# Optimization experiments

Measured on AMD Instinct MI355X. Metric: run time of the kernel, lower is better.

Reference implementation:

```python
import jax, jax.numpy as jnp
import numpy as np

HIDDEN = 2048
ENGRAM = 256
ENTRIES = 32768
K = 3  # conv kernel size
LN_EPS = 1e-6
NORM_EPS = 1e-8
INV_TEMP = ENGRAM ** 0.5  # retrieval_temperature = 1/sqrt(engram_dim)
CLAMP_MIN = 0.5  # step 0 < clamp_until_step=800 -> hard clamp active


def _l2norm(x):
    n = jnp.linalg.norm(x, axis=-1, keepdims=True)
    return x / jnp.maximum(n, NORM_EPS)


def _rmsnorm(x, w, eps=LN_EPS):
    ms = jnp.mean(jnp.square(x), axis=-1, keepdims=True)
    return x * jax.lax.rsqrt(ms + eps) * w


def _layernorm(x, g, b, eps=LN_EPS):
    mu = jnp.mean(x, axis=-1, keepdims=True)
    var = jnp.mean(jnp.square(x - mu), axis=-1, keepdims=True)
    return (x - mu) * jax.lax.rsqrt(var + eps) * g + b


def setup_inputs() -> dict:
    key = jax.random.key(0)
    ks = jax.random.split(key, 7)
    s = lambda fan: 1.0 / np.sqrt(fan)
    return {
        "hidden_state": jax.random.normal(ks[0], (4, 1024, HIDDEN), jnp.float32),
        "table": jax.random.normal(ks[1], (ENTRIES, ENGRAM), jnp.float32),
        "Wq": jax.random.normal(ks[2], (HIDDEN, ENGRAM), jnp.float32) * s(HIDDEN),
        "ln_gamma": jnp.ones((ENGRAM,), jnp.float32),
        "ln_beta": jnp.zeros((ENGRAM,), jnp.float32),
        "Wk": jax.random.normal(ks[3], (ENGRAM, HIDDEN), jnp.float32) * s(ENGRAM),
        "Wv": jax.random.normal(ks[4], (ENGRAM, HIDDEN), jnp.float32) * s(ENGRAM),
        "gate_norm_w": jnp.ones((HIDDEN,), jnp.float32),
        "key_norm_w": jnp.ones((HIDDEN,), jnp.float32),
        # depthwise causal conv weight [C, K] (torch init zeros; randn for a meaningful test)
        "conv_w": jax.random.normal(ks[5], (HIDDEN, K), jnp.float32) * 0.1,
    }


def reference(hidden_state, table, Wq, ln_gamma, ln_beta, Wk, Wv,
              gate_norm_w, key_norm_w, conv_w):
    B, L, C = hidden_state.shape
    # --- retrieval: cosine-sim softmax attention over frozen table ---
    q = jnp.einsum('blc,ce->ble', hidden_state, Wq)
    qn = _l2norm(q)
    tn = _l2norm(table)
    sims = jnp.einsum('ble,te->blt', qn, tn)            # [B,L,T]
    weights = jax.nn.softmax(sims * INV_TEMP, axis=-1)
    retrieved = jnp.einsum('blt,te->ble', weights, table)
    retrieved = _layernorm(retrieved, ln_gamma, ln_beta)
    # --- key/value projections + gating ---
    key_ = jnp.einsum('ble,ec->blc', retrieved, Wk)
    value = jnp.einsum('ble,ec->blc', retrieved, Wv)
    h_norm = _rmsnorm(hidden_state, gate_norm_w)
    k_norm = _rmsnorm(key_, key_norm_w)
    dot = jnp.sum(h_norm * k_norm, axis=-1, keepdims=True)
    raw_gate = jax.nn.sigmoid(dot / np.sqrt(C).astype(np.float32))
    gate = jnp.maximum(raw_gate, CLAMP_MIN)             # clamp phase (step < 800)
    gated = gate * value                                 # [B,L,C]
    # --- causal depthwise conv along seq (left pad K-1) ---
    padded = jnp.pad(gated, ((0, 0), (K - 1, 0), (0, 0)))
    conv = sum(conv_w[:, k] * padded[:, k:k + L, :] for k in range(K))
    return jax.nn.silu(conv), gate
```

## Files before the change

### kernel.cpp

```cpp
#include <hip/hip_runtime.h>
#include <stdint.h>


#define NTOK 4096
#define CDIM 2048
#define EDIM 256
#define TROWS 32768
#define SPLIT 16
#define OUT0 (NTOK * CDIM)

typedef __attribute__((ext_vector_type(8))) short bf16x8;
typedef __attribute__((ext_vector_type(4))) float f32x4;

__device__ inline float bf2f(unsigned short u) { return __uint_as_float((unsigned)u << 16); }
__device__ inline unsigned short f2bf(float f) {
  unsigned x = __float_as_uint(f);
  x += 0x7fffu + ((x >> 16) & 1u);
  return (unsigned short)(x >> 16);
}
__device__ inline unsigned cvt_pk_bf16(float lo, float hi) {
  unsigned r;
  asm("v_cvt_pk_bf16_f32 %0, %1, %2" : "=v"(r) : "v"(lo), "v"(hi));
  return r;
}
__device__ inline void gll16(const void* g, void* l) {
  __builtin_amdgcn_global_load_lds((const __attribute__((address_space(1))) void*)g,
                                   (__attribute__((address_space(3))) void*)l, 16, 0, 0);
}
#define WAIT_VM0() do { asm volatile("s_waitcnt vmcnt(0)" ::: "memory"); \
                        __builtin_amdgcn_sched_barrier(0); } while (0)
#define WAIT_LGKM0() do { asm volatile("s_waitcnt lgkmcnt(0)" ::: "memory"); \
                          __builtin_amdgcn_sched_barrier(0); } while (0)
#define BARRIER() do { __builtin_amdgcn_s_barrier(); \
                       __builtin_amdgcn_sched_barrier(0); } while (0)

__global__ __launch_bounds__(256) void cast_bf16_kernel(
    const float* __restrict__ in, unsigned short* __restrict__ out) {
  const int idx = blockIdx.x * 256 + threadIdx.x;
  float4 v0 = *reinterpret_cast<const float4*>(&in[(size_t)idx * 8]);
  float4 v1 = *reinterpret_cast<const float4*>(&in[(size_t)idx * 8 + 4]);
  bf16x8 o;
  o[0] = (short)f2bf(v0.x); o[1] = (short)f2bf(v0.y);
  o[2] = (short)f2bf(v0.z); o[3] = (short)f2bf(v0.w);
  o[4] = (short)f2bf(v1.x); o[5] = (short)f2bf(v1.y);
  o[6] = (short)f2bf(v1.z); o[7] = (short)f2bf(v1.w);
  *reinterpret_cast<bf16x8*>(&out[(size_t)idx * 8]) = o;
}

__global__ __launch_bounds__(256) void transpose_cast_kernel(
    const float* __restrict__ in0, const float* __restrict__ in1,
    unsigned short* __restrict__ out, int R, int C) {
  __shared__ float lt[32][33];
  const int tid = threadIdx.x;
  const int r0 = blockIdx.x * 32, c0 = blockIdx.y * 32;
  const float* in = blockIdx.z ? in1 : in0;
  unsigned short* op = out + (size_t)blockIdx.z * R * C;
  {
    int r = tid >> 3, c4 = (tid & 7) * 4;
    float4 v = *reinterpret_cast<const float4*>(&in[(size_t)(r0 + r) * C + c0 + c4]);
    lt[r][c4] = v.x; lt[r][c4 + 1] = v.y; lt[r][c4 + 2] = v.z; lt[r][c4 + 3] = v.w;
  }
  __syncthreads();
  {
    int c = tid >> 3, r4 = (tid & 7) * 4;
#pragma unroll
    for (int j = 0; j < 4; ++j)
      op[(size_t)(c0 + c) * R + r0 + r4 + j] = f2bf(lt[r4 + j][c]);
  }
}

__global__ __launch_bounds__(256) void tabprep_kernel(
    const float* __restrict__ table, unsigned short* __restrict__ tnb,
    unsigned short* __restrict__ tvb) {
  __shared__ float lt[32][257];
  __shared__ float inv[32];
  const int tid = threadIdx.x, nb = blockIdx.x;
  const int r0 = nb * 32;
#pragma unroll
  for (int i = 0; i < 8; ++i) {
    int id = i * 256 + tid;
    int row = id >> 6, e4 = (id & 63) * 4;
    float4 v = *reinterpret_cast<const float4*>(&table[(size_t)(r0 + row) * EDIM + e4]);
    lt[row][e4] = v.x; lt[row][e4 + 1] = v.y; lt[row][e4 + 2] = v.z; lt[row][e4 + 3] = v.w;
  }
  __syncthreads();
  {
    int row = tid >> 3, sub = tid & 7;
    float ss = 0.f;
#pragma unroll
    for (int j = 0; j < 32; ++j) { float v = lt[row][sub + 8 * j]; ss = fmaf(v, v, ss); }
    ss += __shfl_xor(ss, 1); ss += __shfl_xor(ss, 2); ss += __shfl_xor(ss, 4);
    if (sub == 0) inv[row] = 1.f / fmaxf(sqrtf(ss), 1e-8f);
  }
  __syncthreads();
#pragma unroll
  for (int i = 0; i < 4; ++i) {
    int q = i * 256 + tid;
    {
      int c8 = q >> 5, row = q & 31;
      bf16x8 v;
#pragma unroll
      for (int j = 0; j < 8; ++j) v[j] = (short)f2bf(lt[row][c8 * 8 + j] * inv[row]);
      *reinterpret_cast<bf16x8*>(&tnb[(size_t)nb * 8192 + q * 8]) = v;
    }
    {
      int hi = q >> 8, e = q & 255;
      bf16x8 v;
#pragma unroll
      for (int j = 0; j < 8; ++j) v[j] = (short)f2bf(lt[hi * 8 + j][e]);
      *reinterpret_cast<bf16x8*>(&tvb[(size_t)nb * 8192 + q * 8]) = v;
    }
  }
}

template <bool F32OUT>
__global__ __launch_bounds__(256, 2) void gemm_bt_kernel(
    const unsigned short* __restrict__ A, const unsigned short* __restrict__ BT,
    void* __restrict__ Cout, int M, int N, int Kfull, int klen) {
  __shared__ alignas(16) unsigned short sA[2][128 * 64];
  __shared__ alignas(16) unsigned short sB[2][128 * 64];
  const int tid = threadIdx.x;
  const int lane = tid & 63;
  const int wave = tid >> 6;
  const int laneLo = lane & 15, laneHi = lane >> 4;
  const int nbn = N >> 7;
  const int bm = blockIdx.x / nbn, bn = blockIdx.x % nbn;
  const int koff = blockIdx.y * klen;
  const int wr = wave >> 1, wc = wave & 1;
  f32x4 acc[4][4];
#pragma unroll
  for (int m = 0; m < 4; ++m)
#pragma unroll
    for (int n = 0; n < 4; ++n) acc[m][n] = (f32x4){0.f, 0.f, 0.f, 0.f};
  const int nkt = klen >> 6;
  auto STAGE = [&](int b, int kt) {
#pragma unroll
    for (int i = 0; i < 4; ++i) {
      int q = i * 256 + tid;
      int row = q >> 3, cl = q & 7;
      int cs = cl ^ (row & 7);
      gll16(A + ((size_t)(bm * 128 + row) * Kfull + koff + kt * 64 + cs * 8), &sA[b][q * 8]);
      gll16(BT + ((size_t)(bn * 128 + row) * Kfull + koff + kt * 64 + cs * 8), &sB[b][q * 8]);
    }
  };
  STAGE(0, 0);
  for (int kt = 0; kt < nkt; ++kt) {
    __syncthreads();
    if (kt + 1 < nkt) STAGE((kt & 1) ^ 1, kt + 1);
    const unsigned short* pA = sA[kt & 1];
    const unsigned short* pB = sB[kt & 1];
#pragma unroll
    for (int ks = 0; ks < 2; ++ks) {
      bf16x8 af[4], bfr[4];
#pragma unroll
      for (int m = 0; m < 4; ++m) {
        int row = wr * 64 + m * 16 + laneLo;
        af[m] = *reinterpret_cast<const bf16x8*>(&pA[(row * 8 + ((ks * 4 + laneHi) ^ (row & 7))) * 8]);
      }
#pragma unroll
      for (int n = 0; n < 4; ++n) {
        int row = wc * 64 + n * 16 + laneLo;
        bfr[n] = *reinterpret_cast<const bf16x8*>(&pB[(row * 8 + ((ks * 4 + laneHi) ^ (row & 7))) * 8]);
      }
#pragma unroll
      for (int m = 0; m < 4; ++m)
#pragma unroll
        for (int n = 0; n < 4; ++n)
          acc[m][n] = __builtin_amdgcn_mfma_f32_16x16x32_bf16(af[m], bfr[n], acc[m][n], 0, 0, 0);
    }
  }
#pragma unroll
  for (int m = 0; m < 4; ++m)
#pragma unroll
    for (int n = 0; n < 4; ++n)
#pragma unroll
      for (int r = 0; r < 4; ++r) {
        size_t idx = (size_t)(bm * 128 + wr * 64 + m * 16 + laneHi * 4 + r) * N +
                     bn * 128 + wc * 64 + n * 16 + laneLo;
        if (F32OUT)
          ((float*)Cout)[(size_t)blockIdx.y * M * N + idx] = acc[m][n][r];
        else
          ((unsigned short*)Cout)[idx] = f2bf(acc[m][n][r]);
      }
}

__global__ __launch_bounds__(256) void qcombine_kernel(
    const float* __restrict__ qpart, unsigned short* __restrict__ qn) {
  __shared__ float red[4];
  const int t = blockIdx.x, e = threadIdx.x;
  const int wave = e >> 6, lane = e & 63;
  float v = qpart[(size_t)t * EDIM + e] + qpart[((size_t)NTOK + t) * EDIM + e];
  float ss = v * v;
#pragma unroll
  for (int m = 1; m <= 32; m <<= 1) ss += __shfl_xor(ss, m);
  if (lane == 0) red[wave] = ss;
  __syncthreads();
  ss = red[0] + red[1] + red[2] + red[3];
  const float inv = 1.f / fmaxf(sqrtf(ss), 1e-8f);
  qn[(size_t)t * EDIM + e] = f2bf(v * inv);
}

__global__ __launch_bounds__(512, 2) void attn_kernel(
    const unsigned short* __restrict__ qn, const unsigned short* __restrict__ tnb,
    const unsigned short* __restrict__ tvb, unsigned short* __restrict__ Opart,
    float* __restrict__ lpart) {
  __shared__ alignas(16) unsigned short bufK[2][8192];
  __shared__ alignas(16) unsigned short bufV[2][8192];
  __shared__ alignas(16) unsigned short pbuf[16][16][40];
  const int tid = threadIdx.x;
  const int wave = tid >> 6, lane = tid & 63;
  const int Lo = lane & 15, Hi = lane >> 4;
  const int cid = (blockIdx.x & 7) * 32 + (blockIdx.x >> 3);
  const int split = cid >> 4, tb = cid & 15;
  const int qkBase = tb * 256 + wave * 32;
  bf16x8 qf[2][8];
#pragma unroll
  for (int g = 0; g < 2; ++g)
#pragma unroll
    for (int ks = 0; ks < 8; ++ks)
      qf[g][ks] = *reinterpret_cast<const bf16x8*>(
          qn + (size_t)(qkBase + g * 16 + Lo) * EDIM + ks * 32 + Hi * 8);
  const int pvG = (wave & 3) * 4;
  const int pvF = (wave >> 2) * 8;
  f32x4 o[4][8];
#pragma unroll
  for (int ng = 0; ng < 4; ++ng)
#pragma unroll
    for (int f = 0; f < 8; ++f) o[ng][f] = (f32x4){0.f, 0.f, 0.f, 0.f};
  float l_run[2] = {0.f, 0.f};
  const int nt = (TROWS / SPLIT) / 32;
  const int nb0 = split * nt;
  auto STAGE = [&](int b, int blk) {
#pragma unroll
    for (int i = 0; i < 2; ++i) {
      gll16(tnb + (size_t)blk * 8192 + (i * 512 + tid) * 8, &bufK[b][(i * 512 + tid) * 8]);
      gll16(tvb + (size_t)blk * 8192 + (i * 512 + tid) * 8, &bufV[b][(i * 512 + tid) * 8]);
    }
  };
  STAGE(0, nb0);
  for (int it = 0; it < nt; ++it) {
    const int cur = it & 1;
    WAIT_VM0();
    WAIT_LGKM0();
    BARRIER();
    if (it + 1 < nt) STAGE(cur ^ 1, nb0 + it + 1);
    f32x4 z00 = {0.f, 0.f, 0.f, 0.f}, z01 = z00, z10 = z00, z11 = z00;
    __builtin_amdgcn_s_setprio(1);
#pragma unroll
    for (int ks = 0; ks < 8; ++ks) {
      bf16x8 a0 = *reinterpret_cast<const bf16x8*>(&bufK[cur][((ks * 4 + Hi) * 32 + Lo) * 8]);
      bf16x8 a1 = *reinterpret_cast<const bf16x8*>(&bufK[cur][((ks * 4 + Hi) * 32 + 16 + Lo) * 8]);
      z00 = __builtin_amdgcn_mfma_f32_16x16x32_bf16(a0, qf[0][ks], z00, 0, 0, 0);
      z01 = __builtin_amdgcn_mfma_f32_16x16x32_bf16(a1, qf[0][ks], z01, 0, 0, 0);
      z10 = __builtin_amdgcn_mfma_f32_16x16x32_bf16(a0, qf[1][ks], z10, 0, 0, 0);
      z11 = __builtin_amdgcn_mfma_f32_16x16x32_bf16(a1, qf[1][ks], z11, 0, 0, 0);
    }
    __builtin_amdgcn_s_setprio(0);
#pragma unroll
    for (int g = 0; g < 2; ++g) {
      const f32x4 za = g ? z10 : z00;
      const f32x4 zb = g ? z11 : z01;
      float p[8];
#pragma unroll
      for (int r = 0; r < 4; ++r) {
        p[r] = __expf(fmaf(16.f, za[r], -16.f));
        p[4 + r] = __expf(fmaf(16.f, zb[r], -16.f));
      }
      l_run[g] += ((p[0] + p[1]) + (p[2] + p[3])) + ((p[4] + p[5]) + (p[6] + p[7]));
      unsigned short* pb = &pbuf[wave * 2 + g][Lo][0];
      *reinterpret_cast<uint2*>(pb + Hi * 4) =
          make_uint2(cvt_pk_bf16(p[0], p[1]), cvt_pk_bf16(p[2], p[3]));
      *reinterpret_cast<uint2*>(pb + 16 + Hi * 4) =
          make_uint2(cvt_pk_bf16(p[4], p[5]), cvt_pk_bf16(p[6], p[7]));
    }
    WAIT_LGKM0();
    BARRIER();
    bf16x8 pa0 = *reinterpret_cast<const bf16x8*>(&pbuf[pvG + 0][Lo][Hi * 8]);
    bf16x8 pa1 = *reinterpret_cast<const bf16x8*>(&pbuf[pvG + 1][Lo][Hi * 8]);
    bf16x8 pa2 = *reinterpret_cast<const bf16x8*>(&pbuf[pvG + 2][Lo][Hi * 8]);
    bf16x8 pa3 = *reinterpret_cast<const bf16x8*>(&pbuf[pvG + 3][Lo][Hi * 8]);
    __builtin_amdgcn_s_setprio(1);
#pragma unroll
    for (int f = 0; f < 8; ++f) {
      bf16x8 vb = *reinterpret_cast<const bf16x8*>(
          &bufV[cur][(Hi * 256 + (pvF + f) * 16 + Lo) * 8]);
      o[0][f] = __builtin_amdgcn_mfma_f32_16x16x32_bf16(pa0, vb, o[0][f], 0, 0, 0);
      o[1][f] = __builtin_amdgcn_mfma_f32_16x16x32_bf16(pa1, vb, o[1][f], 0, 0, 0);
      o[2][f] = __builtin_amdgcn_mfma_f32_16x16x32_bf16(pa2, vb, o[2][f], 0, 0, 0);
      o[3][f] = __builtin_amdgcn_mfma_f32_16x16x32_bf16(pa3, vb, o[3][f], 0, 0, 0);
    }
    __builtin_amdgcn_s_setprio(0);
  }
#pragma unroll
  for (int g = 0; g < 2; ++g) {
    float l = l_run[g];
    l += __shfl_xor(l, 16);
    l += __shfl_xor(l, 32);
    if (lane < 16) lpart[(size_t)split * NTOK + qkBase + g * 16 + Lo] = l;
  }
#pragma unroll
  for (int ng = 0; ng < 4; ++ng)
#pragma unroll
    for (int f = 0; f < 8; ++f)
#pragma unroll
      for (int r = 0; r < 4; ++r) {
        int token = tb * 256 + (pvG + ng) * 16 + Hi * 4 + r;
        Opart[((size_t)split * NTOK + token) * EDIM + (pvF + f) * 16 + Lo] =
            f2bf(o[ng][f][r]);
      }
}

__global__ __launch_bounds__(256) void combine_ln_kernel(
    const unsigned short* __restrict__ Opart, const float* __restrict__ lpart,
    const float* __restrict__ gamma, const float* __restrict__ beta,
    unsigned short* __restrict__ retr) {
  __shared__ float red[4][2];
  const int t = blockIdx.x, e = threadIdx.x;
  const int wave = e >> 6, lane = e & 63;
  float acc = 0.f, l = 0.f;
#pragma unroll
  for (int s = 0; s < SPLIT; ++s) {
    acc += bf2f(Opart[((size_t)s * NTOK + t) * EDIM + e]);
    l += lpart[(size_t)s * NTOK + t];
  }
  const float r = acc / l;
  float s1 = r, s2 = r * r;
#pragma unroll
  for (int m = 1; m <= 32; m <<= 1) { s1 += __shfl_xor(s1, m); s2 += __shfl_xor(s2, m); }
  if (lane == 0) { red[wave][0] = s1; red[wave][1] = s2; }
  __syncthreads();
  s1 = red[0][0] + red[1][0] + red[2][0] + red[3][0];
  s2 = red[0][1] + red[1][1] + red[2][1] + red[3][1];
  const float mu = s1 * (1.f / 256.f);
  const float var = s2 * (1.f / 256.f) - mu * mu;
  const float rs = rsqrtf(var + 1e-6f);
  retr[(size_t)t * EDIM + e] = f2bf((r - mu) * rs * gamma[e] + beta[e]);
}

__global__ __launch_bounds__(256) void gate_kernel(
    const float* __restrict__ hidden, const unsigned short* __restrict__ kv,
    const float* __restrict__ gw, const float* __restrict__ kwn,
    unsigned short* __restrict__ gatedb, float* __restrict__ gate_out) {
  __shared__ float red[4][3];
  const int t = blockIdx.x, tid = threadIdx.x;
  const int wave = tid >> 6, lane = tid & 63;
  float vv[8];
  float ssh = 0.f, ssk = 0.f, shk = 0.f;
#pragma unroll
  for (int i = 0; i < 8; ++i) {
    int cc = tid + i * 256;
    float h = hidden[(size_t)t * CDIM + cc];
    float k = bf2f(kv[(size_t)t * 4096 + cc]);
    vv[i] = bf2f(kv[(size_t)t * 4096 + 2048 + cc]);
    ssh = fmaf(h, h, ssh);
    ssk = fmaf(k, k, ssk);
    shk = fmaf(h * gw[cc], k * kwn[cc], shk);
  }
#pragma unroll
  for (int m = 1; m <= 32; m <<= 1) {
    ssh += __shfl_xor(ssh, m); ssk += __shfl_xor(ssk, m); shk += __shfl_xor(shk, m);
  }
  if (lane == 0) { red[wave][0] = ssh; red[wave][1] = ssk; red[wave][2] = shk; }
  __syncthreads();
  ssh = red[0][0] + red[1][0] + red[2][0] + red[3][0];
  ssk = red[0][1] + red[1][1] + red[2][1] + red[3][1];
  shk = red[0][2] + red[1][2] + red[2][2] + red[3][2];
  const float rsh = rsqrtf(ssh * (1.f / 2048.f) + 1e-6f);
  const float rsk = rsqrtf(ssk * (1.f / 2048.f) + 1e-6f);
  const float dot = rsh * rsk * shk;
  const float rg = 1.f / (1.f + __expf(-dot * 0.02209708691207961f));
  const float gate = fmaxf(rg, 0.5f);
  if (tid == 0) gate_out[t] = gate;
#pragma unroll
  for (int i = 0; i < 8; ++i) {
    int cc = tid + i * 256;
    gatedb[(size_t)t * CDIM + cc] = f2bf(gate * vv[i]);
  }
}

__global__ __launch_bounds__(256) void conv_kernel(
    const unsigned short* __restrict__ gatedb, const float* __restrict__ convw,
    float* __restrict__ out0) {
  const int t = blockIdx.x, tid = threadIdx.x;
  const int l = t & 1023;
  const int c0 = tid * 8;
  bf16x8 gz;
#pragma unroll
  for (int j = 0; j < 8; ++j) gz[j] = 0;
  bf16x8 g2 = *reinterpret_cast<const bf16x8*>(gatedb + (size_t)t * CDIM + c0);
  bf16x8 g1 = (l >= 1) ? *reinterpret_cast<const bf16x8*>(gatedb + (size_t)(t - 1) * CDIM + c0) : gz;
  bf16x8 g0 = (l >= 2) ? *reinterpret_cast<const bf16x8*>(gatedb + (size_t)(t - 2) * CDIM + c0) : gz;
  float res[8];
#pragma unroll
  for (int j = 0; j < 8; ++j) {
    int c = c0 + j;
    float x = convw[c * 3 + 0] * bf2f((unsigned short)g0[j])
            + convw[c * 3 + 1] * bf2f((unsigned short)g1[j])
            + convw[c * 3 + 2] * bf2f((unsigned short)g2[j]);
    res[j] = x / (1.f + __expf(-x));
  }
  *reinterpret_cast<float4*>(out0 + (size_t)t * CDIM + c0) =
      make_float4(res[0], res[1], res[2], res[3]);
  *reinterpret_cast<float4*>(out0 + (size_t)t * CDIM + c0 + 4) =
      make_float4(res[4], res[5], res[6], res[7]);
}

extern "C" void kernel_launch(void* const* d_in, const int* in_sizes, int n_in,
                              void* d_out, int out_size, void* d_ws, size_t ws_size,
                              hipStream_t stream) {
  const float* hidden = (const float*)d_in[0];
  const float* table  = (const float*)d_in[1];
  const float* Wq     = (const float*)d_in[2];
  const float* ln_g   = (const float*)d_in[3];
  const float* ln_b   = (const float*)d_in[4];
  const float* Wk     = (const float*)d_in[5];
  const float* Wv     = (const float*)d_in[6];
  const float* gnw    = (const float*)d_in[7];
  const float* knw    = (const float*)d_in[8];
  const float* convw  = (const float*)d_in[9];
  float* out = (float*)d_out;

  char* w = (char*)d_ws;
  const size_t MB = 1u << 20;
  unsigned short* tnb    = (unsigned short*)(w);
  unsigned short* tvb    = (unsigned short*)(w + 16 * MB);
  unsigned short* kv     = (unsigned short*)(w);
  unsigned short* qn     = (unsigned short*)(w + 32 * MB);
  unsigned short* retr   = (unsigned short*)(w + 32 * MB);
  unsigned short* WkvT   = (unsigned short*)(w + 34 * MB);
  float*          lpart  = (float*)(w + 36 * MB);
  unsigned short* Opart  = (unsigned short*)(w + 37 * MB);
  unsigned short* hb     = (unsigned short*)(w + 37 * MB);
  unsigned short* WqT    = (unsigned short*)(w + 53 * MB);
  float*          qpart  = (float*)(w + 54 * MB);
  unsigned short* gatedb = (unsigned short*)(w + 37 * MB);

  cast_bf16_kernel<<<NTOK * CDIM / 2048, 256, 0, stream>>>(hidden, hb);
  transpose_cast_kernel<<<dim3(64, 8, 1), 256, 0, stream>>>(Wq, Wq, WqT, CDIM, EDIM);
  transpose_cast_kernel<<<dim3(8, 64, 2), 256, 0, stream>>>(Wk, Wv, WkvT, EDIM, CDIM);
  tabprep_kernel<<<TROWS / 32, 256, 0, stream>>>(table, tnb, tvb);
  gemm_bt_kernel<true><<<dim3((NTOK / 128) * (EDIM / 128), 2), 256, 0, stream>>>(
      hb, WqT, qpart, NTOK, EDIM, CDIM, 1024);
  qcombine_kernel<<<NTOK, 256, 0, stream>>>(qpart, qn);
  attn_kernel<<<16 * SPLIT, 512, 0, stream>>>(qn, tnb, tvb, Opart, lpart);
  combine_ln_kernel<<<NTOK, 256, 0, stream>>>(Opart, lpart, ln_g, ln_b, retr);
  gemm_bt_kernel<false><<<dim3((NTOK / 128) * (2 * CDIM / 128), 1), 256, 0, stream>>>(
      retr, WkvT, kv, NTOK, 2 * CDIM, EDIM, EDIM);
  gate_kernel<<<NTOK, 256, 0, stream>>>(hidden, kv, gnw, knw, gatedb, out + OUT0);
  conv_kernel<<<NTOK, 256, 0, stream>>>(gatedb, convw, out);
}
```

Before: 236.6 us.

## Halve attention block size, restage pipeline, fuse gating into conv kernel

The attention kernel drops from 512 to 256 threads per block covering 128 tokens instead of 256, doubling the grid, so each block re-streams the table tiles for fewer queries. The explicit waitcnt/barrier macros are replaced by __syncthreads, and the next-tile prefetch now issues after the score phase rather than before it, which shortens the window for overlapping loads with compute. Separately, the gate kernel no longer writes a gated bf16 intermediate; the conv kernel reads the value half of kv and the per-token gate directly and applies the gate itself, with a remapped token order. This removes one full intermediate write and read but makes the conv kernel read a strided kv layout.

New measurement: 220.3 us. -6.9%, faster.

```diff
diff --git a/kernel.cpp b/kernel.cpp
--- a/kernel.cpp
+++ b/kernel.cpp
@@ -27,12 +27,6 @@
   __builtin_amdgcn_global_load_lds((const __attribute__((address_space(1))) void*)g,
                                    (__attribute__((address_space(3))) void*)l, 16, 0, 0);
 }
-#define WAIT_VM0() do { asm volatile("s_waitcnt vmcnt(0)" ::: "memory"); \
-                        __builtin_amdgcn_sched_barrier(0); } while (0)
-#define WAIT_LGKM0() do { asm volatile("s_waitcnt lgkmcnt(0)" ::: "memory"); \
-                          __builtin_amdgcn_sched_barrier(0); } while (0)
-#define BARRIER() do { __builtin_amdgcn_s_barrier(); \
-                       __builtin_amdgcn_sched_barrier(0); } while (0)
 
 __global__ __launch_bounds__(256) void cast_bf16_kernel(
     const float* __restrict__ in, unsigned short* __restrict__ out) {
@@ -200,19 +194,19 @@
   qn[(size_t)t * EDIM + e] = f2bf(v * inv);
 }
 
-__global__ __launch_bounds__(512, 2) void attn_kernel(
+__global__ __launch_bounds__(256, 2) void attn_kernel(
     const unsigned short* __restrict__ qn, const unsigned short* __restrict__ tnb,
     const unsigned short* __restrict__ tvb, unsigned short* __restrict__ Opart,
     float* __restrict__ lpart) {
   __shared__ alignas(16) unsigned short bufK[2][8192];
   __shared__ alignas(16) unsigned short bufV[2][8192];
-  __shared__ alignas(16) unsigned short pbuf[16][16][40];
+  __shared__ alignas(16) unsigned short pbuf[8][16][40];
   const int tid = threadIdx.x;
   const int wave = tid >> 6, lane = tid & 63;
   const int Lo = lane & 15, Hi = lane >> 4;
-  const int cid = (blockIdx.x & 7) * 32 + (blockIdx.x >> 3);
-  const int split = cid >> 4, tb = cid & 15;
-  const int qkBase = tb * 256 + wave * 32;
+  const int cid = (blockIdx.x & 7) * 64 + (blockIdx.x >> 3);
+  const int split = cid >> 5, tb = cid & 31;
+  const int qkBase = tb * 128 + wave * 32;
   bf16x8 qf[2][8];
 #pragma unroll
   for (int g = 0; g < 2; ++g)
@@ -220,8 +214,8 @@
     for (int ks = 0; ks < 8; ++ks)
       qf[g][ks] = *reinterpret_cast<const bf16x8*>(
           qn + (size_t)(qkBase + g * 16 + Lo) * EDIM + ks * 32 + Hi * 8);
-  const int pvG = (wave & 3) * 4;
-  const int pvF = (wave >> 2) * 8;
+  const int pvG = (wave & 1) * 4;
+  const int pvF = (wave >> 1) * 8;
   f32x4 o[4][8];
 #pragma unroll
   for (int ng = 0; ng < 4; ++ng)
@@ -232,18 +226,16 @@
   const int nb0 = split * nt;
   auto STAGE = [&](int b, int blk) {
 #pragma unroll
-    for (int i = 0; i < 2; ++i) {
-      gll16(tnb + (size_t)blk * 8192 + (i * 512 + tid) * 8, &bufK[b][(i * 512 + tid) * 8]);
-      gll16(tvb + (size_t)blk * 8192 + (i * 512 + tid) * 8, &bufV[b][(i * 512 + tid) * 8]);
+    for (int i = 0; i < 4; ++i) {
+      int u = i * 256 + tid;
+      gll16(tnb + (size_t)blk * 8192 + u * 8, &bufK[b][u * 8]);
+      gll16(tvb + (size_t)blk * 8192 + u * 8, &bufV[b][u * 8]);
     }
   };
   STAGE(0, nb0);
   for (int it = 0; it < nt; ++it) {
     const int cur = it & 1;
-    WAIT_VM0();
-    WAIT_LGKM0();
-    BARRIER();
-    if (it + 1 < nt) STAGE(cur ^ 1, nb0 + it + 1);
+    __syncthreads();
     f32x4 z00 = {0.f, 0.f, 0.f, 0.f}, z01 = z00, z10 = z00, z11 = z00;
     __builtin_amdgcn_s_setprio(1);
 #pragma unroll
@@ -273,8 +265,8 @@
       *reinterpret_cast<uint2*>(pb + 16 + Hi * 4) =
           make_uint2(cvt_pk_bf16(p[4], p[5]), cvt_pk_bf16(p[6], p[7]));
     }
-    WAIT_LGKM0();
-    BARRIER();
+    __syncthreads();
+    if (it + 1 < nt) STAGE(cur ^ 1, nb0 + it + 1);
     bf16x8 pa0 = *reinterpret_cast<const bf16x8*>(&pbuf[pvG + 0][Lo][Hi * 8]);
     bf16x8 pa1 = *reinterpret_cast<const bf16x8*>(&pbuf[pvG + 1][Lo][Hi * 8]);
     bf16x8 pa2 = *reinterpret_cast<const bf16x8*>(&pbuf[pvG + 2][Lo][Hi * 8]);
@@ -304,7 +296,7 @@
     for (int f = 0; f < 8; ++f)
 #pragma unroll
       for (int r = 0; r < 4; ++r) {
-        int token = tb * 256 + (pvG + ng) * 16 + Hi * 4 + r;
+        int token = tb * 128 + (pvG + ng) * 16 + Hi * 4 + r;
         Opart[((size_t)split * NTOK + token) * EDIM + (pvF + f) * 16 + Lo] =
             f2bf(o[ng][f][r]);
       }
@@ -340,18 +332,16 @@
 __global__ __launch_bounds__(256) void gate_kernel(
     const float* __restrict__ hidden, const unsigned short* __restrict__ kv,
     const float* __restrict__ gw, const float* __restrict__ kwn,
-    unsigned short* __restrict__ gatedb, float* __restrict__ gate_out) {
+    float* __restrict__ gate_out) {
   __shared__ float red[4][3];
   const int t = blockIdx.x, tid = threadIdx.x;
   const int wave = tid >> 6, lane = tid & 63;
-  float vv[8];
   float ssh = 0.f, ssk = 0.f, shk = 0.f;
 #pragma unroll
   for (int i = 0; i < 8; ++i) {
     int cc = tid + i * 256;
     float h = hidden[(size_t)t * CDIM + cc];
     float k = bf2f(kv[(size_t)t * 4096 + cc]);
-    vv[i] = bf2f(kv[(size_t)t * 4096 + 2048 + cc]);
     ssh = fmaf(h, h, ssh);
     ssk = fmaf(k, k, ssk);
     shk = fmaf(h * gw[cc], k * kwn[cc], shk);
@@ -369,34 +359,33 @@
   const float rsk = rsqrtf(ssk * (1.f / 2048.f) + 1e-6f);
   const float dot = rsh * rsk * shk;
   const float rg = 1.f / (1.f + __expf(-dot * 0.02209708691207961f));
-  const float gate = fmaxf(rg, 0.5f);
-  if (tid == 0) gate_out[t] = gate;
-#pragma unroll
-  for (int i = 0; i < 8; ++i) {
-    int cc = tid + i * 256;
-    gatedb[(size_t)t * CDIM + cc] = f2bf(gate * vv[i]);
-  }
+  if (tid == 0) gate_out[t] = fmaxf(rg, 0.5f);
 }
 
 __global__ __launch_bounds__(256) void conv_kernel(
-    const unsigned short* __restrict__ gatedb, const float* __restrict__ convw,
-    float* __restrict__ out0) {
-  const int t = blockIdx.x, tid = threadIdx.x;
+    const unsigned short* __restrict__ kv, const float* __restrict__ gate,
+    const float* __restrict__ convw, float* __restrict__ out0) {
+  const int bid = blockIdx.x, tid = threadIdx.x;
+  const int t = (bid & 7) * 512 + (bid >> 3);
   const int l = t & 1023;
   const int c0 = tid * 8;
-  bf16x8 gz;
-#pragma unroll
-  for (int j = 0; j < 8; ++j) gz[j] = 0;
-  bf16x8 g2 = *reinterpret_cast<const bf16x8*>(gatedb + (size_t)t * CDIM + c0);
-  bf16x8 g1 = (l >= 1) ? *reinterpret_cast<const bf16x8*>(gatedb + (size_t)(t - 1) * CDIM + c0) : gz;
-  bf16x8 g0 = (l >= 2) ? *reinterpret_cast<const bf16x8*>(gatedb + (size_t)(t - 2) * CDIM + c0) : gz;
+  const float gt2 = gate[t];
+  const float gt1 = (l >= 1) ? gate[t - 1] : 0.f;
+  const float gt0 = (l >= 2) ? gate[t - 2] : 0.f;
+  bf16x8 vz;
+#pragma unroll
+  for (int j = 0; j < 8; ++j) vz[j] = 0;
+  const unsigned short* vbase = kv + 2048;
+  bf16x8 v2 = *reinterpret_cast<const bf16x8*>(vbase + (size_t)t * 4096 + c0);
+  bf16x8 v1 = (l >= 1) ? *reinterpret_cast<const bf16x8*>(vbase + (size_t)(t - 1) * 4096 + c0) : vz;
+  bf16x8 v0 = (l >= 2) ? *reinterpret_cast<const bf16x8*>(vbase + (size_t)(t - 2) * 4096 + c0) : vz;
   float res[8];
 #pragma unroll
   for (int j = 0; j < 8; ++j) {
     int c = c0 + j;
-    float x = convw[c * 3 + 0] * bf2f((unsigned short)g0[j])
-            + convw[c * 3 + 1] * bf2f((unsigned short)g1[j])
-            + convw[c * 3 + 2] * bf2f((unsigned short)g2[j]);
+    float x = convw[c * 3 + 0] * (gt0 * bf2f((unsigned short)v0[j]))
+            + convw[c * 3 + 1] * (gt1 * bf2f((unsigned short)v1[j]))
+            + convw[c * 3 + 2] * (gt2 * bf2f((unsigned short)v2[j]));
     res[j] = x / (1.f + __expf(-x));
   }
   *reinterpret_cast<float4*>(out0 + (size_t)t * CDIM + c0) =
@@ -433,7 +422,6 @@
   unsigned short* hb     = (unsigned short*)(w + 37 * MB);
   unsigned short* WqT    = (unsigned short*)(w + 53 * MB);
   float*          qpart  = (float*)(w + 54 * MB);
-  unsigned short* gatedb = (unsigned short*)(w + 37 * MB);
 
   cast_bf16_kernel<<<NTOK * CDIM / 2048, 256, 0, stream>>>(hidden, hb);
   transpose_cast_kernel<<<dim3(64, 8, 1), 256, 0, stream>>>(Wq, Wq, WqT, CDIM, EDIM);
@@ -442,10 +430,10 @@
   gemm_bt_kernel<true><<<dim3((NTOK / 128) * (EDIM / 128), 2), 256, 0, stream>>>(
       hb, WqT, qpart, NTOK, EDIM, CDIM, 1024);
   qcombine_kernel<<<NTOK, 256, 0, stream>>>(qpart, qn);
-  attn_kernel<<<16 * SPLIT, 512, 0, stream>>>(qn, tnb, tvb, Opart, lpart);
+  attn_kernel<<<32 * SPLIT, 256, 0, stream>>>(qn, tnb, tvb, Opart, lpart);
   combine_ln_kernel<<<NTOK, 256, 0, stream>>>(Opart, lpart, ln_g, ln_b, retr);
   gemm_bt_kernel<false><<<dim3((NTOK / 128) * (2 * CDIM / 128), 1), 256, 0, stream>>>(
       retr, WkvT, kv, NTOK, 2 * CDIM, EDIM, EDIM);
-  gate_kernel<<<NTOK, 256, 0, stream>>>(hidden, kv, gnw, knw, gatedb, out + OUT0);
-  conv_kernel<<<NTOK, 256, 0, stream>>>(gatedb, convw, out);
-}
+  gate_kernel<<<NTOK, 256, 0, stream>>>(hidden, kv, gnw, knw, out + OUT0);
+  conv_kernel<<<NTOK, 256, 0, stream>>>(kv, out + OUT0, convw, out);
+}
```
